# Optimization experiments

Hardware: AMD Instinct MI355X
Metric: run time of the kernel (lower is better)

Reference implementation:

```python
import jax, jax.numpy as jnp
import numpy as np

NBINS = 256  # skimage threshold_otsu default
RGB_W = np.array([0.2989, 0.5870, 0.1140], dtype=np.float32)  # tf.image.rgb_to_grayscale weights


def setup_inputs() -> dict:
    key = jax.random.key(0)
    inputs = jax.random.uniform(key, (16, 1024, 1024, 3), dtype=jnp.float32)
    return {"inputs": inputs}


def _otsu_threshold(x_flat):
    # Histogram over [min, max] with NBINS bins (skimage semantics: one
    # global threshold over the whole array passed to threshold_otsu).
    mn = x_flat.min()
    mx = x_flat.max()
    width = (mx - mn) / NBINS
    idx = jnp.clip(((x_flat - mn) / width).astype(jnp.int32), 0, NBINS - 1)
    counts = jnp.zeros((NBINS,), jnp.float32).at[idx].add(1.0)
    centers = mn + width * (jnp.arange(NBINS, dtype=jnp.float32) + 0.5)

    # class-separation (between-class variance) per candidate split
    w1 = jnp.cumsum(counts)                      # weight of class 1 (<= t)
    w2 = jnp.cumsum(counts[::-1])[::-1]          # weight of class 2 (> t)
    s1 = jnp.cumsum(counts * centers)
    s2 = jnp.cumsum((counts * centers)[::-1])[::-1]
    m1 = s1 / jnp.maximum(w1, 1.0)
    m2 = s2 / jnp.maximum(w2, 1.0)
    var12 = w1[:-1] * w2[1:] * (m1[:-1] - m2[1:]) ** 2
    return centers[jnp.argmax(var12)]


def reference(inputs):
    # rgb -> grayscale (tf.image.rgb_to_grayscale weights), keep channel dim
    gray = jnp.einsum('bhwc,c->bhw', inputs[..., :3], jnp.asarray(RGB_W))[..., None]
    thresh = _otsu_threshold(gray.ravel())  # single global threshold over the whole batch
    return jnp.where(gray > thresh, 1.0, 0.0).astype(jnp.float32)
```

## Files before the change

kernel.cpp:

```cpp
#include <hip/hip_runtime.h>


static constexpr float W0 = 0.2989f;
static constexpr float W1 = 0.5870f;
static constexpr float W2 = 0.1140f;

static constexpr int GRAY_BLOCKS = 4096;
static constexpr int HIST_BLOCKS = 512;
static constexpr int BIN_BLOCKS  = 1024;

__device__ __forceinline__ float gray_of(float r, float g, float b) {
    return __fadd_rn(__fadd_rn(__fmul_rn(r, W0), __fmul_rn(g, W1)), __fmul_rn(b, W2));
}

__device__ __forceinline__ void wave_minmax(float& lmin, float& lmax) {
    #pragma unroll
    for (int off = 32; off > 0; off >>= 1) {
        lmin = fminf(lmin, __shfl_down(lmin, off));
        lmax = fmaxf(lmax, __shfl_down(lmax, off));
    }
}

__device__ __forceinline__ void reduce_partials(
        const float* __restrict__ pmin, const float* __restrict__ pmax,
        int n, float& out_mn, float& out_mx) {
    __shared__ float smin[4], smax[4];
    int t = threadIdx.x;
    float lmin = __uint_as_float(0x7f800000u);
    float lmax = -lmin;
    for (int i = t; i < n; i += 256) {
        lmin = fminf(lmin, pmin[i]);
        lmax = fmaxf(lmax, pmax[i]);
    }
    wave_minmax(lmin, lmax);
    if ((t & 63) == 0) { smin[t >> 6] = lmin; smax[t >> 6] = lmax; }
    __syncthreads();
    out_mn = fminf(fminf(smin[0], smin[1]), fminf(smin[2], smin[3]));
    out_mx = fmaxf(fmaxf(smax[0], smax[1]), fmaxf(smax[2], smax[3]));
    __syncthreads();
}

__global__ __launch_bounds__(256) void k_gray(
        const float4* __restrict__ in4, float4* __restrict__ gray4,
        float* __restrict__ pmin, float* __restrict__ pmax, int ntiles) {
    __shared__ float4 sv[768];
    int t = threadIdx.x;
    float lmin = __uint_as_float(0x7f800000u);
    float lmax = -lmin;
    for (int tile = blockIdx.x; tile < ntiles; tile += gridDim.x) {
        const float4* src = in4 + (size_t)tile * 768;
        float4 v0 = src[t];
        float4 v1 = src[t + 256];
        float4 v2 = src[t + 512];
        __syncthreads();
        sv[t] = v0; sv[t + 256] = v1; sv[t + 512] = v2;
        __syncthreads();
        float4 a = sv[3 * t + 0];
        float4 b = sv[3 * t + 1];
        float4 c = sv[3 * t + 2];
        float g0 = gray_of(a.x, a.y, a.z);
        float g1 = gray_of(a.w, b.x, b.y);
        float g2 = gray_of(b.z, b.w, c.x);
        float g3 = gray_of(c.y, c.z, c.w);
        float4 o; o.x = g0; o.y = g1; o.z = g2; o.w = g3;
        gray4[(size_t)tile * 256 + t] = o;
        lmin = fminf(lmin, fminf(fminf(g0, g1), fminf(g2, g3)));
        lmax = fmaxf(lmax, fmaxf(fmaxf(g0, g1), fmaxf(g2, g3)));
    }
    wave_minmax(lmin, lmax);
    __shared__ float smin[4], smax[4];
    if ((t & 63) == 0) { smin[t >> 6] = lmin; smax[t >> 6] = lmax; }
    __syncthreads();
    if (t == 0) {
        pmin[blockIdx.x] = fminf(fminf(smin[0], smin[1]), fminf(smin[2], smin[3]));
        pmax[blockIdx.x] = fmaxf(fmaxf(smax[0], smax[1]), fmaxf(smax[2], smax[3]));
    }
}

__global__ __launch_bounds__(256) void k_hist(
        const float4* __restrict__ gray4,
        const float* __restrict__ pmin, const float* __restrict__ pmax,
        unsigned* __restrict__ hist_part, int npix4) {
    float mn, mx;
    reduce_partials(pmin, pmax, GRAY_BLOCKS, mn, mx);
    float width = __fdiv_rn(__fsub_rn(mx, mn), 256.0f);

    __shared__ unsigned lh[1024];
    for (int j = threadIdx.x; j < 1024; j += 256) lh[j] = 0u;
    __syncthreads();
    unsigned* myh = &lh[(threadIdx.x >> 6) << 8];
    int stride = gridDim.x * 256;
    for (int i = blockIdx.x * 256 + threadIdx.x; i < npix4; i += stride) {
        float4 g = gray4[i];
        int i0 = (int)__fdiv_rn(__fsub_rn(g.x, mn), width);
        int i1 = (int)__fdiv_rn(__fsub_rn(g.y, mn), width);
        int i2 = (int)__fdiv_rn(__fsub_rn(g.z, mn), width);
        int i3 = (int)__fdiv_rn(__fsub_rn(g.w, mn), width);
        i0 = min(max(i0, 0), 255);
        i1 = min(max(i1, 0), 255);
        i2 = min(max(i2, 0), 255);
        i3 = min(max(i3, 0), 255);
        atomicAdd(&myh[i0], 1u);
        atomicAdd(&myh[i1], 1u);
        atomicAdd(&myh[i2], 1u);
        atomicAdd(&myh[i3], 1u);
    }
    __syncthreads();
    int b = threadIdx.x;
    hist_part[(size_t)blockIdx.x * 256 + b] =
        lh[b] + lh[256 + b] + lh[512 + b] + lh[768 + b];
}

__global__ __launch_bounds__(256) void k_bin(
        float4* __restrict__ g4,
        const float* __restrict__ pmin, const float* __restrict__ pmax,
        const unsigned* __restrict__ hist_part, int npix4) {
    float mn, mx;
    reduce_partials(pmin, pmax, GRAY_BLOCKS, mn, mx);
    float width = __fdiv_rn(__fsub_rn(mx, mn), 256.0f);

    __shared__ float counts[256], centers[256], tt[256];
    __shared__ float w1[256], s1[256], w2[256], s2[256], vv[256];
    __shared__ float s_th;
    int t = threadIdx.x;

    unsigned c = 0;
    #pragma unroll 8
    for (int k = 0; k < HIST_BLOCKS; ++k)
        c += hist_part[(size_t)k * 256 + t];
    counts[t] = (float)c;
    centers[t] = __fadd_rn(mn, __fmul_rn(width, __fadd_rn((float)t, 0.5f)));
    tt[t] = __fmul_rn(counts[t], centers[t]);
    __syncthreads();
    if (t == 0) {
        float aw = 0.0f, as = 0.0f;
        #pragma unroll 16
        for (int i = 0; i < 256; ++i) {
            aw = __fadd_rn(aw, counts[i]); w1[i] = aw;
            as = __fadd_rn(as, tt[i]);     s1[i] = as;
        }
        aw = 0.0f; as = 0.0f;
        #pragma unroll 16
        for (int i = 255; i >= 0; --i) {
            aw = __fadd_rn(aw, counts[i]); w2[i] = aw;
            as = __fadd_rn(as, tt[i]);     s2[i] = as;
        }
    }
    __syncthreads();
    if (t < 255) {
        float m1 = __fdiv_rn(s1[t],     fmaxf(w1[t],     1.0f));
        float m2 = __fdiv_rn(s2[t + 1], fmaxf(w2[t + 1], 1.0f));
        float d  = __fsub_rn(m1, m2);
        vv[t] = __fmul_rn(__fmul_rn(w1[t], w2[t + 1]), __fmul_rn(d, d));
    }
    __syncthreads();
    if (t == 0) {
        float best = -1.0f; int bi = 0;
        #pragma unroll 16
        for (int i = 0; i < 255; ++i) {
            float v = vv[i];
            if (v > best) { best = v; bi = i; }
        }
        s_th = centers[bi];
    }
    __syncthreads();
    const float th = s_th;

    int stride = gridDim.x * 256;
    for (int i = blockIdx.x * 256 + t; i < npix4; i += stride) {
        float4 g = g4[i];
        float4 o;
        o.x = g.x > th ? 1.0f : 0.0f;
        o.y = g.y > th ? 1.0f : 0.0f;
        o.z = g.z > th ? 1.0f : 0.0f;
        o.w = g.w > th ? 1.0f : 0.0f;
        g4[i] = o;
    }
}

extern "C" void kernel_launch(void* const* d_in, const int* in_sizes, int n_in,
                              void* d_out, int out_size, void* d_ws, size_t ws_size,
                              hipStream_t stream) {
    const float4* in4 = (const float4*)d_in[0];
    float4* gray4 = (float4*)d_out;

    int npix = in_sizes[0] / 3;
    int npix4 = npix / 4;
    int ntiles = npix / 1024;

    float* pmin = (float*)d_ws;
    float* pmax = pmin + GRAY_BLOCKS;
    unsigned* hist_part = (unsigned*)(pmax + GRAY_BLOCKS);

    k_gray<<<GRAY_BLOCKS, 256, 0, stream>>>(in4, gray4, pmin, pmax, ntiles);
    k_hist<<<HIST_BLOCKS, 256, 0, stream>>>((const float4*)d_out, pmin, pmax,
                                            hist_part, npix4);
    k_bin<<<BIN_BLOCKS, 256, 0, stream>>>(gray4, pmin, pmax, hist_part, npix4);
}
```

Before: 371.9 us.

## Compute Otsu threshold once in a dedicated kernel and simplify gray/bin kernels

Moves the histogram merge and Otsu threshold search out of every binarize block into a single 1024-thread kernel that writes the threshold to workspace. Before, each of the 1024 k_bin blocks re-read all 512 partial histograms and ran the serial scans. The gray kernel drops its LDS transpose and reads three float4s per thread directly. Binarize now runs one-shot blocks over fixed 1024-float4 chunks. This adds a kernel launch and a serial single-block stage, and assumes the pixel count is an exact multiple of the block tile.

Measured after the change: 357.8 us. 1.04x faster.

```diff
diff --git a/kernel.cpp b/kernel.cpp
--- a/kernel.cpp
+++ b/kernel.cpp
@@ -7,7 +7,7 @@
 
 static constexpr int GRAY_BLOCKS = 4096;
 static constexpr int HIST_BLOCKS = 512;
-static constexpr int BIN_BLOCKS  = 1024;
+static constexpr int BIN_BLOCKS  = 4096;
 
 __device__ __forceinline__ float gray_of(float r, float g, float b) {
     return __fadd_rn(__fadd_rn(__fmul_rn(r, W0), __fmul_rn(g, W1)), __fmul_rn(b, W2));
@@ -23,47 +23,45 @@
 
 __device__ __forceinline__ void reduce_partials(
         const float* __restrict__ pmin, const float* __restrict__ pmax,
-        int n, float& out_mn, float& out_mx) {
-    __shared__ float smin[4], smax[4];
+        int n, int nthreads, float& out_mn, float& out_mx) {
+    __shared__ float smin[16], smax[16];
     int t = threadIdx.x;
     float lmin = __uint_as_float(0x7f800000u);
     float lmax = -lmin;
-    for (int i = t; i < n; i += 256) {
+    for (int i = t; i < n; i += nthreads) {
         lmin = fminf(lmin, pmin[i]);
         lmax = fmaxf(lmax, pmax[i]);
     }
     wave_minmax(lmin, lmax);
+    int nw = nthreads >> 6;
     if ((t & 63) == 0) { smin[t >> 6] = lmin; smax[t >> 6] = lmax; }
     __syncthreads();
-    out_mn = fminf(fminf(smin[0], smin[1]), fminf(smin[2], smin[3]));
-    out_mx = fmaxf(fmaxf(smax[0], smax[1]), fmaxf(smax[2], smax[3]));
+    float m = smin[0], M = smax[0];
+    for (int w = 1; w < nw; ++w) { m = fminf(m, smin[w]); M = fmaxf(M, smax[w]); }
+    out_mn = m; out_mx = M;
     __syncthreads();
 }
 
 __global__ __launch_bounds__(256) void k_gray(
         const float4* __restrict__ in4, float4* __restrict__ gray4,
-        float* __restrict__ pmin, float* __restrict__ pmax, int ntiles) {
-    __shared__ float4 sv[768];
-    int t = threadIdx.x;
+        float* __restrict__ pmin, float* __restrict__ pmax) {
+    int t = threadIdx.x;
+    int base = blockIdx.x * 1024;
     float lmin = __uint_as_float(0x7f800000u);
     float lmax = -lmin;
-    for (int tile = blockIdx.x; tile < ntiles; tile += gridDim.x) {
-        const float4* src = in4 + (size_t)tile * 768;
-        float4 v0 = src[t];
-        float4 v1 = src[t + 256];
-        float4 v2 = src[t + 512];
-        __syncthreads();
-        sv[t] = v0; sv[t + 256] = v1; sv[t + 512] = v2;
-        __syncthreads();
-        float4 a = sv[3 * t + 0];
-        float4 b = sv[3 * t + 1];
-        float4 c = sv[3 * t + 2];
+    #pragma unroll
+    for (int j = 0; j < 4; ++j) {
+        int g = base + j * 256 + t;
+        const float4* src = in4 + 3 * (size_t)g;
+        float4 a = src[0];
+        float4 b = src[1];
+        float4 c = src[2];
         float g0 = gray_of(a.x, a.y, a.z);
         float g1 = gray_of(a.w, b.x, b.y);
         float g2 = gray_of(b.z, b.w, c.x);
         float g3 = gray_of(c.y, c.z, c.w);
         float4 o; o.x = g0; o.y = g1; o.z = g2; o.w = g3;
-        gray4[(size_t)tile * 256 + t] = o;
+        gray4[g] = o;
         lmin = fminf(lmin, fminf(fminf(g0, g1), fminf(g2, g3)));
         lmax = fmaxf(lmax, fmaxf(fmaxf(g0, g1), fmaxf(g2, g3)));
     }
@@ -82,7 +80,7 @@
         const float* __restrict__ pmin, const float* __restrict__ pmax,
         unsigned* __restrict__ hist_part, int npix4) {
     float mn, mx;
-    reduce_partials(pmin, pmax, GRAY_BLOCKS, mn, mx);
+    reduce_partials(pmin, pmax, GRAY_BLOCKS, 256, mn, mx);
     float width = __fdiv_rn(__fsub_rn(mx, mn), 256.0f);
 
     __shared__ unsigned lh[1024];
@@ -111,26 +109,31 @@
         lh[b] + lh[256 + b] + lh[512 + b] + lh[768 + b];
 }
 
-__global__ __launch_bounds__(256) void k_bin(
-        float4* __restrict__ g4,
+__global__ __launch_bounds__(1024) void k_otsu(
+        const unsigned* __restrict__ hist_part,
         const float* __restrict__ pmin, const float* __restrict__ pmax,
-        const unsigned* __restrict__ hist_part, int npix4) {
+        float* __restrict__ thresh) {
     float mn, mx;
-    reduce_partials(pmin, pmax, GRAY_BLOCKS, mn, mx);
+    reduce_partials(pmin, pmax, GRAY_BLOCKS, 1024, mn, mx);
     float width = __fdiv_rn(__fsub_rn(mx, mn), 256.0f);
 
+    __shared__ unsigned csum[1024];
     __shared__ float counts[256], centers[256], tt[256];
     __shared__ float w1[256], s1[256], w2[256], s2[256], vv[256];
-    __shared__ float s_th;
-    int t = threadIdx.x;
-
-    unsigned c = 0;
+    int t = threadIdx.x;
+    int b = t & 255, q = t >> 8;
+    unsigned acc = 0;
     #pragma unroll 8
-    for (int k = 0; k < HIST_BLOCKS; ++k)
-        c += hist_part[(size_t)k * 256 + t];
-    counts[t] = (float)c;
-    centers[t] = __fadd_rn(mn, __fmul_rn(width, __fadd_rn((float)t, 0.5f)));
-    tt[t] = __fmul_rn(counts[t], centers[t]);
+    for (int k = q; k < HIST_BLOCKS; k += 4)
+        acc += hist_part[(size_t)k * 256 + b];
+    csum[q * 256 + b] = acc;
+    __syncthreads();
+    if (t < 256) {
+        unsigned c = csum[t] + csum[256 + t] + csum[512 + t] + csum[768 + t];
+        counts[t] = (float)c;
+        centers[t] = __fadd_rn(mn, __fmul_rn(width, __fadd_rn((float)t, 0.5f)));
+        tt[t] = __fmul_rn(counts[t], centers[t]);
+    }
     __syncthreads();
     if (t == 0) {
         float aw = 0.0f, as = 0.0f;
@@ -161,13 +164,18 @@
             float v = vv[i];
             if (v > best) { best = v; bi = i; }
         }
-        s_th = centers[bi];
-    }
-    __syncthreads();
-    const float th = s_th;
-
-    int stride = gridDim.x * 256;
-    for (int i = blockIdx.x * 256 + t; i < npix4; i += stride) {
+        *thresh = centers[bi];
+    }
+}
+
+__global__ __launch_bounds__(256) void k_bin(
+        float4* __restrict__ g4, const float* __restrict__ thresh) {
+    const float th = thresh[0];
+    int t = threadIdx.x;
+    int base = blockIdx.x * 1024;
+    #pragma unroll
+    for (int j = 0; j < 4; ++j) {
+        int i = base + j * 256 + t;
         float4 g = g4[i];
         float4 o;
         o.x = g.x > th ? 1.0f : 0.0f;
@@ -186,14 +194,15 @@
 
     int npix = in_sizes[0] / 3;
     int npix4 = npix / 4;
-    int ntiles = npix / 1024;
 
     float* pmin = (float*)d_ws;
     float* pmax = pmin + GRAY_BLOCKS;
-    unsigned* hist_part = (unsigned*)(pmax + GRAY_BLOCKS);
-
-    k_gray<<<GRAY_BLOCKS, 256, 0, stream>>>(in4, gray4, pmin, pmax, ntiles);
+    float* thresh = pmax + GRAY_BLOCKS;
+    unsigned* hist_part = (unsigned*)(thresh + 1);
+
+    k_gray<<<GRAY_BLOCKS, 256, 0, stream>>>(in4, gray4, pmin, pmax);
     k_hist<<<HIST_BLOCKS, 256, 0, stream>>>((const float4*)d_out, pmin, pmax,
                                             hist_part, npix4);
-    k_bin<<<BIN_BLOCKS, 256, 0, stream>>>(gray4, pmin, pmax, hist_part, npix4);
-}
+    k_otsu<<<1, 1024, 0, stream>>>(hist_part, pmin, pmax, thresh);
+    k_bin<<<BIN_BLOCKS, 256, 0, stream>>>(gray4, thresh);
+}
```
